# Performance work log

Measured on AMD Instinct MI355X. Metric: run time of the kernel, lower is better.

Reference implementation:

```python
import jax, jax.numpy as jnp
import numpy as np

N, E = 20000, 160000
F, H, OUT = 256, 8, 128
L = 6            # total layers -> 5 GAT layers
LM1 = L - 1
NGN = L // 3 + 1 # 3 GraphNorms
D = F // H       # 32 per head
GN_FREQ = 3
EPS = 1e-5


def setup_inputs() -> dict:
    key = jax.random.key(0)
    ks = jax.random.split(key, 12)
    x = jax.random.normal(ks[0], (N, 1), dtype=jnp.float32)
    edge_index = jax.random.randint(ks[1], (2, E), 0, N, dtype=jnp.int32)
    W0 = jax.random.normal(ks[2], (1, F), dtype=jnp.float32) * 0.1
    b0 = jnp.zeros((F,), jnp.float32)
    gat_lin = jax.random.normal(ks[3], (LM1, F, F), dtype=jnp.float32) * (1.0 / np.sqrt(F))
    att_src = jax.random.normal(ks[4], (LM1, H, D), dtype=jnp.float32) * 0.1
    att_dst = jax.random.normal(ks[5], (LM1, H, D), dtype=jnp.float32) * 0.1
    gat_bias = jnp.zeros((LM1, F), jnp.float32)
    gn_weight = jnp.ones((NGN, F), jnp.float32)
    gn_bias = jnp.zeros((NGN, F), jnp.float32)
    gn_mean_scale = jnp.ones((NGN, F), jnp.float32)
    lin_W = jax.random.normal(ks[6], (F, OUT), dtype=jnp.float32) * (1.0 / np.sqrt(F))
    lin_b = jnp.zeros((OUT,), jnp.float32)
    return {"x": x, "W0": W0, "b0": b0, "gat_lin": gat_lin, "att_src": att_src,
            "att_dst": att_dst, "gat_bias": gat_bias, "gn_weight": gn_weight,
            "gn_bias": gn_bias, "gn_mean_scale": gn_mean_scale,
            "lin_W": lin_W, "lin_b": lin_b, "edge_index": edge_index}


def _gcn_conv(x, W, b, src, dst, n):
    h = x @ W
    deg = jax.ops.segment_sum(jnp.ones(src.shape[0], h.dtype), dst, num_segments=n)
    dinv = jnp.where(deg > 0, jax.lax.rsqrt(deg), 0.0)
    norm = dinv[src] * dinv[dst]                      # [E']
    out = jax.ops.segment_sum(h[src] * norm[:, None], dst, num_segments=n)
    return out + b


def _gat_conv(x, W, a_src, a_dst, src, dst, n):
    # PyG GATConv (concat=True, negative_slope=0.2, self-loops in src/dst)
    h = (x @ W).reshape(n, H, D)
    s = jnp.einsum('nhd,hd->nh', h, a_src)            # [N,H]
    t = jnp.einsum('nhd,hd->nh', h, a_dst)
    e = jax.nn.leaky_relu(s[src] + t[dst], 0.2)       # [E',H]
    m = jax.ops.segment_max(e, dst, num_segments=n)   # per-dst softmax
    e = jnp.exp(e - m[dst])
    denom = jax.ops.segment_sum(e, dst, num_segments=n)
    alpha = e / (denom[dst] + 1e-16)
    out = jax.ops.segment_sum(h[src] * alpha[:, :, None], dst, num_segments=n)
    return out.reshape(n, F)


def _graph_norm(x, w, b, ms):
    # PyG GraphNorm with batch=None (single graph): per-feature stats over nodes
    mean = jnp.mean(x, axis=0)
    out = x - ms * mean
    var = jnp.mean(out * out, axis=0)
    return w * out * jax.lax.rsqrt(var + EPS) + b


def reference(x, W0, b0, gat_lin, att_src, att_dst, gat_bias, gn_weight, gn_bias,
              gn_mean_scale, lin_W, lin_b, edge_index):
    n = x.shape[0]
    loops = jnp.arange(n, dtype=edge_index.dtype)
    src = jnp.concatenate([edge_index[0], loops])
    dst = jnp.concatenate([edge_index[1], loops])
    h = jax.nn.relu(_gcn_conv(x, W0, b0, src, dst, n))
    for i in range(LM1):
        if i % GN_FREQ == 0:
            g = i // GN_FREQ
            h = _graph_norm(h, gn_weight[g], gn_bias[g], gn_mean_scale[g])
        out = _gat_conv(h, gat_lin[i], att_src[i], att_dst[i], src, dst, n)
        if i % GN_FREQ == 0:
            out = out + gat_bias[i]
        h = h + jax.nn.relu(out)
    return h @ lin_W + lin_b
```

## Files before the change

### kernel.cpp

```cpp
#include <hip/hip_runtime.h>
#include <hip/hip_bf16.h>
#include <stdint.h>

typedef float f32x4 __attribute__((ext_vector_type(4)));
typedef short s16x8 __attribute__((ext_vector_type(8)));

__device__ __forceinline__ float bf2f(unsigned short u) {
    union { unsigned int i; float f; } v; v.i = ((unsigned int)u) << 16; return v.f;
}
__device__ __forceinline__ unsigned short f2bf(float f) {
    union { float f; unsigned int i; } v; v.f = f;
    unsigned int x = v.i;
    return (unsigned short)((x + 0x7fffu + ((x >> 16) & 1u)) >> 16);
}
__device__ __forceinline__ void gload16(const void* g, void* l) {
    __builtin_amdgcn_global_load_lds(
        (const __attribute__((address_space(1))) void*)g,
        (__attribute__((address_space(3))) void*)l, 16, 0, 0);
}

__global__ void k_count(const int* __restrict__ ei, int E, int* deg) {
    int e = blockIdx.x * blockDim.x + threadIdx.x;
    if (e < E) atomicAdd(&deg[ei[E + e]], 1);
}

__global__ __launch_bounds__(256) void k_bsum(const int* __restrict__ deg,
                                              int* __restrict__ bsum, int n) {
    __shared__ int buf[256];
    int i = blockIdx.x * 256 + threadIdx.x;
    buf[threadIdx.x] = (i < n) ? deg[i] + 1 : 0;
    __syncthreads();
#pragma unroll
    for (int off = 128; off > 0; off >>= 1) {
        if ((int)threadIdx.x < off) buf[threadIdx.x] += buf[threadIdx.x + off];
        __syncthreads();
    }
    if (threadIdx.x == 0) bsum[blockIdx.x] = buf[0];
}

__global__ __launch_bounds__(256) void k_scanb(const int* __restrict__ bsum,
                                               int* __restrict__ boff, int nb) {
    __shared__ int buf[256];
    int t = threadIdx.x;
    int v = (t < nb) ? bsum[t] : 0;
    buf[t] = v;
    __syncthreads();
    for (int off = 1; off < 256; off <<= 1) {
        int add = (t >= off) ? buf[t - off] : 0;
        __syncthreads();
        buf[t] += add;
        __syncthreads();
    }
    if (t < nb) boff[t] = buf[t] - v;
}

__global__ __launch_bounds__(256) void k_emit(const int* __restrict__ deg,
                                              const int* __restrict__ boff,
                                              int* __restrict__ rowptr,
                                              int* __restrict__ wo,
                                              float* __restrict__ dinv, int n) {
    __shared__ int buf[256];
    int i = blockIdx.x * 256 + threadIdx.x;
    int v = (i < n) ? deg[i] + 1 : 0;
    buf[threadIdx.x] = v;
    __syncthreads();
    for (int off = 1; off < 256; off <<= 1) {
        int add = ((int)threadIdx.x >= off) ? buf[threadIdx.x - off] : 0;
        __syncthreads();
        buf[threadIdx.x] += add;
        __syncthreads();
    }
    if (i < n) {
        int excl = boff[blockIdx.x] + buf[threadIdx.x] - v;
        rowptr[i] = excl;
        wo[i] = excl;
        dinv[i] = rsqrtf((float)v);
        if (i == n - 1) rowptr[n] = excl + v;
    }
}

__global__ void k_fill(const int* __restrict__ ei, int E, int n,
                       int* wo, int* srcs) {
    int e = blockIdx.x * blockDim.x + threadIdx.x;
    int EP = E + n;
    if (e >= EP) return;
    int s_, d_;
    if (e < E) { s_ = ei[e]; d_ = ei[E + e]; }
    else       { s_ = d_ = e - E; }
    int pos = atomicAdd(&wo[d_], 1);
    srcs[pos] = s_;
}

__global__ __launch_bounds__(256) void k_h0f(const float* __restrict__ x,
                                             const float* __restrict__ dinv,
                                             const int* __restrict__ rowptr,
                                             const int* __restrict__ srcs,
                                             const float* __restrict__ W0,
                                             const float* __restrict__ b0,
                                             unsigned short* __restrict__ hbf,
                                             int n, int Mpad) {
    int wave = threadIdx.x >> 6, lane = threadIdx.x & 63;
    int node = blockIdx.x * 4 + wave;
    if (node >= Mpad) return;
    size_t base = (size_t)node * 256 + lane * 4;
    if (node >= n) {
        ushort4 z = {0, 0, 0, 0};
        *reinterpret_cast<ushort4*>(hbf + base) = z;
        return;
    }
    int p0 = rowptr[node], p1 = rowptr[node + 1];
    float sum = 0.f;
    for (int p = p0 + lane; p < p1; p += 64) {
        int s = srcs[p];
        sum += x[s] * dinv[s];
    }
#pragma unroll
    for (int m = 1; m < 64; m <<= 1) sum += __shfl_xor(sum, m);
    float sv = sum * dinv[node];
    float4 wv = *reinterpret_cast<const float4*>(W0 + lane * 4);
    float4 bv = *reinterpret_cast<const float4*>(b0 + lane * 4);
    ushort4 o;
    o.x = f2bf(fmaxf(sv * wv.x + bv.x, 0.f));
    o.y = f2bf(fmaxf(sv * wv.y + bv.y, 0.f));
    o.z = f2bf(fmaxf(sv * wv.z + bv.z, 0.f));
    o.w = f2bf(fmaxf(sv * wv.w + bv.w, 0.f));
    *reinterpret_cast<ushort4*>(hbf + base) = o;
}

__global__ void k_wprep(const float* __restrict__ gat_lin,
                        const float* __restrict__ lin_W,
                        const float* __restrict__ att_src,
                        const float* __restrict__ att_dst,
                        unsigned short* __restrict__ Wt,
                        unsigned short* __restrict__ lt) {
    int idx = blockIdx.x * blockDim.x + threadIdx.x;
    const int T1 = 5 * 65536;
    const int T2 = T1 + 128 * 256;
    const int T3 = T2 + 5 * 64 * 256;
    if (idx < T1) {
        int l = idx >> 16, r = idx & 0xFFFF;
        int nrow = r >> 8, k = r & 255;
        Wt[(size_t)l * 81920 + nrow * 256 + k] =
            f2bf(gat_lin[(size_t)l * 65536 + k * 256 + nrow]);
    } else if (idx < T2) {
        int j = idx - T1;
        int nrow = j >> 8, k = j & 255;
        lt[nrow * 256 + k] = f2bf(lin_W[(size_t)k * 128 + nrow]);
    } else if (idx < T3) {
        int j = idx - T2;
        int l = j >> 14, r = j & 16383;
        int row = r >> 8, k = r & 255;
        float v = 0.f;
        if (row < 16) {
            int head = row & 7;
            const float* a = (row < 8) ? (att_src + l * 256 + head * 32)
                                       : (att_dst + l * 256 + head * 32);
            const float* wr = gat_lin + (size_t)l * 65536 + k * 256 + head * 32;
#pragma unroll
            for (int d = 0; d < 32; ++d) v += wr[d] * a[d];
        }
        Wt[(size_t)l * 81920 + (256 + row) * 256 + k] = f2bf(v);
    }
}

__global__ __launch_bounds__(256) void k_gn_reduce(const unsigned short* __restrict__ hbf,
                                                   float* sums, float* sumsq, int n) {
    int f = threadIdx.x;
    float s = 0.f, q = 0.f;
    for (int r = blockIdx.x; r < n; r += gridDim.x) {
        float v = bf2f(hbf[(size_t)r * 256 + f]);
        s += v; q += v * v;
    }
    atomicAdd(&sums[f], s);
    atomicAdd(&sumsq[f], q);
}

__global__ __launch_bounds__(256) void k_gnfold(const float* __restrict__ st,
                                                const float* __restrict__ w,
                                                const float* __restrict__ b,
                                                const float* __restrict__ ms,
                                                unsigned short* __restrict__ Wt,
                                                float* __restrict__ so,
                                                float* __restrict__ rowbias,
                                                float ninv) {
    __shared__ float red[256];
    int col = blockIdx.x, k = threadIdx.x;
    float mean = st[k] * ninv;
    float m2   = st[256 + k] * ninv;
    float msf  = ms[k];
    float var  = m2 + msf * mean * mean * (msf - 2.0f);
    float sc = w[k] * rsqrtf(var + 1e-5f);
    float of = b[k] - msf * mean * sc;
    size_t idx = (size_t)col * 256 + k;
    float wv = bf2f(Wt[idx]);
    red[k] = of * wv;
    __syncthreads();
#pragma unroll
    for (int off = 128; off > 0; off >>= 1) {
        if (k < off) red[k] += red[k + off];
        __syncthreads();
    }
    if (k == 0) rowbias[col] = red[0];
    Wt[idx] = f2bf(sc * wv);
    if (col == 0) { so[k] = sc; so[256 + k] = of; }
}

#define BM 64
__global__ __launch_bounds__(512) void k_gemm_mfma(
    const unsigned short* __restrict__ A,
    const unsigned short* __restrict__ Bt,
    unsigned short* __restrict__ Cb,
    float* __restrict__ Cf,
    float* __restrict__ sbuf,
    float* __restrict__ tbuf,
    const float* __restrict__ bias,
    const float* __restrict__ rowbias,
    int M, int ldc, int nbTot, int nbPerY)
{
    __shared__ unsigned short As[64 * 256];
    __shared__ unsigned short Bs[2][64 * 256];
    const int tid = threadIdx.x;
    const int bm = blockIdx.x * BM;
    const int nb0 = blockIdx.y * nbPerY;
    int nb1 = nb0 + nbPerY; if (nb1 > nbTot) nb1 = nbTot;

    {
        const char* ga = (const char*)(A + (size_t)bm * 256);
        const char* gb = (const char*)(Bt + (size_t)nb0 * 16384);
        char* la = (char*)As;
        char* lb = (char*)Bs[0];
#pragma unroll
        for (int i = 0; i < 4; ++i) {
            int o  = (i * 512 + tid) * 16;
            int so = o ^ (((o >> 9) & 7) << 4);
            gload16(ga + so, la + o);
            gload16(gb + so, lb + o);
        }
    }
    __syncthreads();

    const int lane = tid & 63;
    const int w  = tid >> 6;
    const int wm = (w >> 1) * 16;
    const int wn = (w & 1) * 32;
    const int r  = lane & 15, kb = lane >> 4;
    const int r4 = (lane >> 4) * 4, cc = lane & 15;
    const char* la = (const char*)As;

    for (int nb = nb0; nb < nb1; ++nb) {
        int cur = (nb - nb0) & 1;
        if (nb + 1 < nb1) {
            const char* gb = (const char*)(Bt + (size_t)(nb + 1) * 16384);
            char* lb = (char*)Bs[cur ^ 1];
#pragma unroll
            for (int i = 0; i < 4; ++i) {
                int o  = (i * 512 + tid) * 16;
                int so = o ^ (((o >> 9) & 7) << 4);
                gload16(gb + so, lb + o);
            }
        }
        const char* lb = (const char*)Bs[cur];
        f32x4 acc[2] = {};
#pragma unroll
        for (int ks = 0; ks < 8; ++ks) {
            int row = wm + r;
            int c16 = (ks * 4 + kb) ^ (row & 7);
            s16x8 af = *(const s16x8*)(la + row * 512 + c16 * 16);
#pragma unroll
            for (int j = 0; j < 2; ++j) {
                int col = wn + j * 16 + r;
                int d16 = (ks * 4 + kb) ^ (col & 7);
                s16x8 bfr = *(const s16x8*)(lb + col * 512 + d16 * 16);
                acc[j] = __builtin_amdgcn_mfma_f32_16x16x32_bf16(af, bfr, acc[j], 0, 0, 0);
            }
        }
#pragma unroll
        for (int j = 0; j < 2; ++j) {
            int col = nb * 64 + wn + j * 16 + cc;
            float rb = rowbias ? rowbias[col] : 0.f;
#pragma unroll
            for (int q = 0; q < 4; ++q) {
                int row = bm + wm + r4 + q;
                float v = acc[j][q] + rb;
                if (Cb) {
                    if (col < 256) {
                        Cb[(size_t)row * 256 + col] = f2bf(v);
                    } else if (col < 264) {
                        sbuf[(size_t)row * 8 + (col - 256)] = v;
                    } else if (col < 272) {
                        tbuf[(size_t)row * 8 + (col - 264)] = v;
                    }
                } else if (row < M) {
                    Cf[(size_t)row * ldc + col] = v + bias[col];
                }
            }
        }
        __syncthreads();
    }
}

__global__ __launch_bounds__(256) void k_fagg(const unsigned short* __restrict__ h1,
                                              const float* __restrict__ sbuf,
                                              const float* __restrict__ tbuf,
                                              const int* __restrict__ rowptr,
                                              const int* __restrict__ srcs,
                                              unsigned short* __restrict__ hbf,
                                              const float* __restrict__ bias,
                                              const float* __restrict__ so, int n) {
    int wave = threadIdx.x >> 6, lane = threadIdx.x & 63;
    int node = blockIdx.x * 4 + wave;
    if (node >= n) return;
    int p0 = rowptr[node], p1 = rowptr[node + 1];
    int head = lane >> 3;
    float tv = tbuf[node * 8 + head];
    float m = -1e30f, den = 0.f;
    float a0 = 0.f, a1 = 0.f, a2 = 0.f, a3 = 0.f;
    int p = p0;
    for (; p + 3 < p1; p += 4) {
        int s0 = srcs[p], s1 = srcs[p + 1], s2 = srcs[p + 2], s3 = srcs[p + 3];
        float e0 = sbuf[s0 * 8 + head] + tv;
        float e1 = sbuf[s1 * 8 + head] + tv;
        float e2 = sbuf[s2 * 8 + head] + tv;
        float e3 = sbuf[s3 * 8 + head] + tv;
        ushort4 v0 = reinterpret_cast<const ushort4*>(h1 + (size_t)s0 * 256)[lane];
        ushort4 v1 = reinterpret_cast<const ushort4*>(h1 + (size_t)s1 * 256)[lane];
        ushort4 v2 = reinterpret_cast<const ushort4*>(h1 + (size_t)s2 * 256)[lane];
        ushort4 v3 = reinterpret_cast<const ushort4*>(h1 + (size_t)s3 * 256)[lane];
        e0 = (e0 > 0.f) ? e0 : 0.2f * e0;
        e1 = (e1 > 0.f) ? e1 : 0.2f * e1;
        e2 = (e2 > 0.f) ? e2 : 0.2f * e2;
        e3 = (e3 > 0.f) ? e3 : 0.2f * e3;
        float em = fmaxf(fmaxf(e0, e1), fmaxf(e2, e3));
        float mn = fmaxf(m, em);
        float sc = __expf(m - mn);
        float w0 = __expf(e0 - mn), w1 = __expf(e1 - mn);
        float w2 = __expf(e2 - mn), w3 = __expf(e3 - mn);
        den = den * sc + ((w0 + w1) + (w2 + w3));
        a0 = fmaf(a0, sc, w0 * bf2f(v0.x) + w1 * bf2f(v1.x) + w2 * bf2f(v2.x) + w3 * bf2f(v3.x));
        a1 = fmaf(a1, sc, w0 * bf2f(v0.y) + w1 * bf2f(v1.y) + w2 * bf2f(v2.y) + w3 * bf2f(v3.y));
        a2 = fmaf(a2, sc, w0 * bf2f(v0.z) + w1 * bf2f(v1.z) + w2 * bf2f(v2.z) + w3 * bf2f(v3.z));
        a3 = fmaf(a3, sc, w0 * bf2f(v0.w) + w1 * bf2f(v1.w) + w2 * bf2f(v2.w) + w3 * bf2f(v3.w));
        m = mn;
    }
    for (; p < p1; ++p) {
        int s0 = srcs[p];
        float e0 = sbuf[s0 * 8 + head] + tv;
        e0 = (e0 > 0.f) ? e0 : 0.2f * e0;
        ushort4 v0 = reinterpret_cast<const ushort4*>(h1 + (size_t)s0 * 256)[lane];
        float mn = fmaxf(m, e0);
        float sc = __expf(m - mn);
        float w0 = __expf(e0 - mn);
        den = den * sc + w0;
        a0 = fmaf(a0, sc, w0 * bf2f(v0.x));
        a1 = fmaf(a1, sc, w0 * bf2f(v0.y));
        a2 = fmaf(a2, sc, w0 * bf2f(v0.z));
        a3 = fmaf(a3, sc, w0 * bf2f(v0.w));
        m = mn;
    }
    float inv = 1.0f / (den + 1e-16f);
    a0 *= inv; a1 *= inv; a2 *= inv; a3 *= inv;
    float b0_ = 0.f, b1_ = 0.f, b2_ = 0.f, b3_ = 0.f;
    if (bias) {
        float4 bb = reinterpret_cast<const float4*>(bias)[lane];
        b0_ = bb.x; b1_ = bb.y; b2_ = bb.z; b3_ = bb.w;
    }
    size_t base = (size_t)node * 256 + lane * 4;
    ushort4 hv = *reinterpret_cast<const ushort4*>(hbf + base);
    float h0 = bf2f(hv.x), h1v = bf2f(hv.y), h2 = bf2f(hv.z), h3 = bf2f(hv.w);
    if (so) {
        float4 sc4 = reinterpret_cast<const float4*>(so)[lane];
        float4 of4 = reinterpret_cast<const float4*>(so + 256)[lane];
        h0 = h0 * sc4.x + of4.x; h1v = h1v * sc4.y + of4.y;
        h2 = h2 * sc4.z + of4.z; h3 = h3 * sc4.w + of4.w;
    }
    ushort4 o;
    o.x = f2bf(h0  + fmaxf(a0 + b0_, 0.f));
    o.y = f2bf(h1v + fmaxf(a1 + b1_, 0.f));
    o.z = f2bf(h2  + fmaxf(a2 + b2_, 0.f));
    o.w = f2bf(h3  + fmaxf(a3 + b3_, 0.f));
    *reinterpret_cast<ushort4*>(hbf + base) = o;
}

extern "C" void kernel_launch(void* const* d_in, const int* in_sizes, int n_in,
                              void* d_out, int out_size, void* d_ws, size_t ws_size,
                              hipStream_t stream) {
    const float* x        = (const float*)d_in[0];
    const float* W0       = (const float*)d_in[1];
    const float* b0       = (const float*)d_in[2];
    const float* gat_lin  = (const float*)d_in[3];
    const float* att_src  = (const float*)d_in[4];
    const float* att_dst  = (const float*)d_in[5];
    const float* gat_bias = (const float*)d_in[6];
    const float* gn_w     = (const float*)d_in[7];
    const float* gn_b     = (const float*)d_in[8];
    const float* gn_ms    = (const float*)d_in[9];
    const float* lin_W    = (const float*)d_in[10];
    const float* lin_b    = (const float*)d_in[11];
    const int*   ei       = (const int*)d_in[12];

    const int n  = in_sizes[0];
    const int E  = in_sizes[12] / 2;
    const int EP = E + n;
    const int Mpad = ((n + BM - 1) / BM) * BM;
    const int nb = (n + 255) / 256;

    char* w = (char*)d_ws;
    unsigned short* hbf = (unsigned short*)w; w += (size_t)Mpad * 256 * 2;
    unsigned short* h1  = (unsigned short*)w; w += (size_t)Mpad * 256 * 2;
    float* sbuf = (float*)w;                  w += (size_t)Mpad * 8 * 4;
    float* tbuf = (float*)w;                  w += (size_t)Mpad * 8 * 4;
    unsigned short* Wt = (unsigned short*)w;  w += (size_t)5 * 320 * 256 * 2;
    unsigned short* lt = (unsigned short*)w;  w += (size_t)128 * 256 * 2;
    float* scaleoff = (float*)w;              w += 1024 * 4;
    float* rowbias  = (float*)w;              w += 640 * 4;
    float* gnstat = (float*)w;                w += 1024 * 4;
    int* deg    = (int*)w;                    w += (size_t)n * 4;
    float* dinv = (float*)w;                  w += (size_t)n * 4;
    int* rowptr = (int*)w;                    w += ((size_t)(n + 1) * 4 + 15) / 16 * 16;
    int* wo     = (int*)w;                    w += (size_t)n * 4;
    int* bsum   = (int*)w;                    w += ((size_t)nb * 4 + 15) / 16 * 16;
    int* boff   = (int*)w;                    w += ((size_t)nb * 4 + 15) / 16 * 16;
    int* srcs   = (int*)w;                    w += (size_t)EP * 4;

    const int B256 = 256;
    auto cdiv = [](int a, int b) { return (a + b - 1) / b; };

    hipMemsetAsync(gnstat, 0, 1024 * 4 + (size_t)n * 4, stream);

    const int WPREP = 5 * 65536 + 128 * 256 + 5 * 64 * 256;
    k_wprep<<<cdiv(WPREP, B256), B256, 0, stream>>>(gat_lin, lin_W, att_src, att_dst, Wt, lt);

    k_count<<<cdiv(E, B256), B256, 0, stream>>>(ei, E, deg);
    k_bsum<<<nb, 256, 0, stream>>>(deg, bsum, n);
    k_scanb<<<1, 256, 0, stream>>>(bsum, boff, nb);
    k_emit<<<nb, 256, 0, stream>>>(deg, boff, rowptr, wo, dinv, n);
    k_fill<<<cdiv(EP, B256), B256, 0, stream>>>(ei, E, n, wo, srcs);

    k_h0f<<<cdiv(Mpad, 4), 256, 0, stream>>>(x, dinv, rowptr, srcs, W0, b0, hbf, n, Mpad);

    const float ninv = 1.0f / (float)n;
    const int gx = Mpad / BM;

    for (int i = 0; i < 5; ++i) {
        const float* rb = nullptr;
        const float* so = nullptr;
        if (i % 3 == 0) {
            int g = i / 3;
            k_gn_reduce<<<256, 256, 0, stream>>>(hbf, gnstat + g * 512,
                                                 gnstat + g * 512 + 256, n);
            k_gnfold<<<320, 256, 0, stream>>>(gnstat + g * 512, gn_w + g * 256,
                                              gn_b + g * 256, gn_ms + g * 256,
                                              Wt + (size_t)i * 81920,
                                              scaleoff + g * 512, rowbias + g * 320, ninv);
            rb = rowbias + g * 320;
            so = scaleoff + g * 512;
        }
        k_gemm_mfma<<<dim3(gx, 2), 512, 0, stream>>>(
            hbf, Wt + (size_t)i * 81920, h1, nullptr, sbuf, tbuf, nullptr, rb,
            n, 256, 5, 3);
        k_fagg<<<cdiv(n, 4), 256, 0, stream>>>(
            h1, sbuf, tbuf, rowptr, srcs, hbf,
            (i % 3 == 0) ? gat_bias + i * 256 : nullptr, so, n);
    }

    k_gemm_mfma<<<dim3(gx, 1), 512, 0, stream>>>(
        hbf, lt, nullptr, (float*)d_out, nullptr, nullptr, lin_b, nullptr,
        n, 128, 2, 2);
}
```

Before: 309.1 us.

## Split GEMM into one N-tile per block and halve-wave edge split in aggregation

The GEMM now gives each block a single 64-column output tile via a larger grid, which removes the double-buffered B loop and halves B's LDS footprint. That brings more parallelism and occupancy at the cost of reloading the A tile once per column tile. The aggregation kernel splits each node's edges across the two half-waves. Each lane loads 16 bytes (8 bf16) per edge, and the two halves merge their online-softmax state with cross-lane shuffles. This gives more independent gathers in flight and wider loads, but half the lanes sit idle during the epilogue.

```diff
diff --git a/kernel.cpp b/kernel.cpp
--- a/kernel.cpp
+++ b/kernel.cpp
@@ -12,6 +12,11 @@
     union { float f; unsigned int i; } v; v.f = f;
     unsigned int x = v.i;
     return (unsigned short)((x + 0x7fffu + ((x >> 16) & 1u)) >> 16);
+}
+__device__ __forceinline__ void bfp(unsigned int u, float& lo, float& hi) {
+    union { unsigned int i; float f; } a, b;
+    a.i = u << 16; b.i = u & 0xffff0000u;
+    lo = a.f; hi = b.f;
 }
 __device__ __forceinline__ void gload16(const void* g, void* l) {
     __builtin_amdgcn_global_load_lds(
@@ -215,20 +220,18 @@
     float* __restrict__ tbuf,
     const float* __restrict__ bias,
     const float* __restrict__ rowbias,
-    int M, int ldc, int nbTot, int nbPerY)
+    int M, int ldc)
 {
     __shared__ unsigned short As[64 * 256];
-    __shared__ unsigned short Bs[2][64 * 256];
+    __shared__ unsigned short Bs[64 * 256];
     const int tid = threadIdx.x;
     const int bm = blockIdx.x * BM;
-    const int nb0 = blockIdx.y * nbPerY;
-    int nb1 = nb0 + nbPerY; if (nb1 > nbTot) nb1 = nbTot;
-
+    const int bn = blockIdx.y * 64;
     {
         const char* ga = (const char*)(A + (size_t)bm * 256);
-        const char* gb = (const char*)(Bt + (size_t)nb0 * 16384);
+        const char* gb = (const char*)(Bt + (size_t)bn * 256);
         char* la = (char*)As;
-        char* lb = (char*)Bs[0];
+        char* lb = (char*)Bs;
 #pragma unroll
         for (int i = 0; i < 4; ++i) {
             int o  = (i * 512 + tid) * 16;
@@ -246,56 +249,42 @@
     const int r  = lane & 15, kb = lane >> 4;
     const int r4 = (lane >> 4) * 4, cc = lane & 15;
     const char* la = (const char*)As;
-
-    for (int nb = nb0; nb < nb1; ++nb) {
-        int cur = (nb - nb0) & 1;
-        if (nb + 1 < nb1) {
-            const char* gb = (const char*)(Bt + (size_t)(nb + 1) * 16384);
-            char* lb = (char*)Bs[cur ^ 1];
-#pragma unroll
-            for (int i = 0; i < 4; ++i) {
-                int o  = (i * 512 + tid) * 16;
-                int so = o ^ (((o >> 9) & 7) << 4);
-                gload16(gb + so, lb + o);
+    const char* lb = (const char*)Bs;
+
+    f32x4 acc[2] = {};
+#pragma unroll
+    for (int ks = 0; ks < 8; ++ks) {
+        int row = wm + r;
+        int c16 = (ks * 4 + kb) ^ (row & 7);
+        s16x8 af = *(const s16x8*)(la + row * 512 + c16 * 16);
+#pragma unroll
+        for (int j = 0; j < 2; ++j) {
+            int col = wn + j * 16 + r;
+            int d16 = (ks * 4 + kb) ^ (col & 7);
+            s16x8 bfr = *(const s16x8*)(lb + col * 512 + d16 * 16);
+            acc[j] = __builtin_amdgcn_mfma_f32_16x16x32_bf16(af, bfr, acc[j], 0, 0, 0);
+        }
+    }
+#pragma unroll
+    for (int j = 0; j < 2; ++j) {
+        int col = bn + wn + j * 16 + cc;
+        float rb = rowbias ? rowbias[col] : 0.f;
+#pragma unroll
+        for (int q = 0; q < 4; ++q) {
+            int row = bm + wm + r4 + q;
+            float v = acc[j][q] + rb;
+            if (Cb) {
+                if (col < 256) {
+                    Cb[(size_t)row * 256 + col] = f2bf(v);
+                } else if (col < 264) {
+                    sbuf[(size_t)row * 8 + (col - 256)] = v;
+                } else if (col < 272) {
+                    tbuf[(size_t)row * 8 + (col - 264)] = v;
+                }
+            } else if (row < M) {
+                Cf[(size_t)row * ldc + col] = v + bias[col];
             }
         }
-        const char* lb = (const char*)Bs[cur];
-        f32x4 acc[2] = {};
-#pragma unroll
-        for (int ks = 0; ks < 8; ++ks) {
-            int row = wm + r;
-            int c16 = (ks * 4 + kb) ^ (row & 7);
-            s16x8 af = *(const s16x8*)(la + row * 512 + c16 * 16);
-#pragma unroll
-            for (int j = 0; j < 2; ++j) {
-                int col = wn + j * 16 + r;
-                int d16 = (ks * 4 + kb) ^ (col & 7);
-                s16x8 bfr = *(const s16x8*)(lb + col * 512 + d16 * 16);
-                acc[j] = __builtin_amdgcn_mfma_f32_16x16x32_bf16(af, bfr, acc[j], 0, 0, 0);
-            }
-        }
-#pragma unroll
-        for (int j = 0; j < 2; ++j) {
-            int col = nb * 64 + wn + j * 16 + cc;
-            float rb = rowbias ? rowbias[col] : 0.f;
-#pragma unroll
-            for (int q = 0; q < 4; ++q) {
-                int row = bm + wm + r4 + q;
-                float v = acc[j][q] + rb;
-                if (Cb) {
-                    if (col < 256) {
-                        Cb[(size_t)row * 256 + col] = f2bf(v);
-                    } else if (col < 264) {
-                        sbuf[(size_t)row * 8 + (col - 256)] = v;
-                    } else if (col < 272) {
-                        tbuf[(size_t)row * 8 + (col - 264)] = v;
-                    }
-                } else if (row < M) {
-                    Cf[(size_t)row * ldc + col] = v + bias[col];
-                }
-            }
-        }
-        __syncthreads();
     }
 }
 
@@ -311,74 +300,114 @@
     int node = blockIdx.x * 4 + wave;
     if (node >= n) return;
     int p0 = rowptr[node], p1 = rowptr[node + 1];
-    int head = lane >> 3;
+    int hid = lane >> 5;
+    int l5 = lane & 31;
+    int fl = l5 * 8;
+    int head = l5 >> 2;
     float tv = tbuf[node * 8 + head];
     float m = -1e30f, den = 0.f;
     float a0 = 0.f, a1 = 0.f, a2 = 0.f, a3 = 0.f;
-    int p = p0;
-    for (; p + 3 < p1; p += 4) {
-        int s0 = srcs[p], s1 = srcs[p + 1], s2 = srcs[p + 2], s3 = srcs[p + 3];
+    float a4 = 0.f, a5 = 0.f, a6 = 0.f, a7 = 0.f;
+    int q = p0 + hid;
+    for (; q + 2 < p1; q += 4) {
+        int s0 = srcs[q], s1 = srcs[q + 2];
         float e0 = sbuf[s0 * 8 + head] + tv;
         float e1 = sbuf[s1 * 8 + head] + tv;
-        float e2 = sbuf[s2 * 8 + head] + tv;
-        float e3 = sbuf[s3 * 8 + head] + tv;
-        ushort4 v0 = reinterpret_cast<const ushort4*>(h1 + (size_t)s0 * 256)[lane];
-        ushort4 v1 = reinterpret_cast<const ushort4*>(h1 + (size_t)s1 * 256)[lane];
-        ushort4 v2 = reinterpret_cast<const ushort4*>(h1 + (size_t)s2 * 256)[lane];
-        ushort4 v3 = reinterpret_cast<const ushort4*>(h1 + (size_t)s3 * 256)[lane];
+        uint4 v0 = *reinterpret_cast<const uint4*>(h1 + (size_t)s0 * 256 + fl);
+        uint4 v1 = *reinterpret_cast<const uint4*>(h1 + (size_t)s1 * 256 + fl);
         e0 = (e0 > 0.f) ? e0 : 0.2f * e0;
         e1 = (e1 > 0.f) ? e1 : 0.2f * e1;
-        e2 = (e2 > 0.f) ? e2 : 0.2f * e2;
-        e3 = (e3 > 0.f) ? e3 : 0.2f * e3;
-        float em = fmaxf(fmaxf(e0, e1), fmaxf(e2, e3));
-        float mn = fmaxf(m, em);
+        float mn = fmaxf(m, fmaxf(e0, e1));
         float sc = __expf(m - mn);
         float w0 = __expf(e0 - mn), w1 = __expf(e1 - mn);
-        float w2 = __expf(e2 - mn), w3 = __expf(e3 - mn);
-        den = den * sc + ((w0 + w1) + (w2 + w3));
-        a0 = fmaf(a0, sc, w0 * bf2f(v0.x) + w1 * bf2f(v1.x) + w2 * bf2f(v2.x) + w3 * bf2f(v3.x));
-        a1 = fmaf(a1, sc, w0 * bf2f(v0.y) + w1 * bf2f(v1.y) + w2 * bf2f(v2.y) + w3 * bf2f(v3.y));
-        a2 = fmaf(a2, sc, w0 * bf2f(v0.z) + w1 * bf2f(v1.z) + w2 * bf2f(v2.z) + w3 * bf2f(v3.z));
-        a3 = fmaf(a3, sc, w0 * bf2f(v0.w) + w1 * bf2f(v1.w) + w2 * bf2f(v2.w) + w3 * bf2f(v3.w));
+        den = den * sc + (w0 + w1);
+        float f0l, f0h, f1l, f1h;
+        bfp(v0.x, f0l, f0h); bfp(v1.x, f1l, f1h);
+        a0 = fmaf(a0, sc, w0 * f0l + w1 * f1l);
+        a1 = fmaf(a1, sc, w0 * f0h + w1 * f1h);
+        bfp(v0.y, f0l, f0h); bfp(v1.y, f1l, f1h);
+        a2 = fmaf(a2, sc, w0 * f0l + w1 * f1l);
+        a3 = fmaf(a3, sc, w0 * f0h + w1 * f1h);
+        bfp(v0.z, f0l, f0h); bfp(v1.z, f1l, f1h);
+        a4 = fmaf(a4, sc, w0 * f0l + w1 * f1l);
+        a5 = fmaf(a5, sc, w0 * f0h + w1 * f1h);
+        bfp(v0.w, f0l, f0h); bfp(v1.w, f1l, f1h);
+        a6 = fmaf(a6, sc, w0 * f0l + w1 * f1l);
+        a7 = fmaf(a7, sc, w0 * f0h + w1 * f1h);
         m = mn;
     }
-    for (; p < p1; ++p) {
-        int s0 = srcs[p];
+    for (; q < p1; q += 2) {
+        int s0 = srcs[q];
         float e0 = sbuf[s0 * 8 + head] + tv;
+        uint4 v0 = *reinterpret_cast<const uint4*>(h1 + (size_t)s0 * 256 + fl);
         e0 = (e0 > 0.f) ? e0 : 0.2f * e0;
-        ushort4 v0 = reinterpret_cast<const ushort4*>(h1 + (size_t)s0 * 256)[lane];
         float mn = fmaxf(m, e0);
         float sc = __expf(m - mn);
         float w0 = __expf(e0 - mn);
         den = den * sc + w0;
-        a0 = fmaf(a0, sc, w0 * bf2f(v0.x));
-        a1 = fmaf(a1, sc, w0 * bf2f(v0.y));
-        a2 = fmaf(a2, sc, w0 * bf2f(v0.z));
-        a3 = fmaf(a3, sc, w0 * bf2f(v0.w));
+        float f0l, f0h;
+        bfp(v0.x, f0l, f0h);
+        a0 = fmaf(a0, sc, w0 * f0l); a1 = fmaf(a1, sc, w0 * f0h);
+        bfp(v0.y, f0l, f0h);
+        a2 = fmaf(a2, sc, w0 * f0l); a3 = fmaf(a3, sc, w0 * f0h);
+        bfp(v0.z, f0l, f0h);
+        a4 = fmaf(a4, sc, w0 * f0l); a5 = fmaf(a5, sc, w0 * f0h);
+        bfp(v0.w, f0l, f0h);
+        a6 = fmaf(a6, sc, w0 * f0l); a7 = fmaf(a7, sc, w0 * f0h);
         m = mn;
     }
+    float mo = __shfl_xor(m, 32);
+    float mm = fmaxf(m, mo);
+    float sc = __expf(m - mm);
+    den *= sc; den += __shfl_xor(den, 32);
+    a0 *= sc; a0 += __shfl_xor(a0, 32);
+    a1 *= sc; a1 += __shfl_xor(a1, 32);
+    a2 *= sc; a2 += __shfl_xor(a2, 32);
+    a3 *= sc; a3 += __shfl_xor(a3, 32);
+    a4 *= sc; a4 += __shfl_xor(a4, 32);
+    a5 *= sc; a5 += __shfl_xor(a5, 32);
+    a6 *= sc; a6 += __shfl_xor(a6, 32);
+    a7 *= sc; a7 += __shfl_xor(a7, 32);
+    if (hid) return;
     float inv = 1.0f / (den + 1e-16f);
     a0 *= inv; a1 *= inv; a2 *= inv; a3 *= inv;
-    float b0_ = 0.f, b1_ = 0.f, b2_ = 0.f, b3_ = 0.f;
+    a4 *= inv; a5 *= inv; a6 *= inv; a7 *= inv;
+    float b_[8] = {0.f, 0.f, 0.f, 0.f, 0.f, 0.f, 0.f, 0.f};
     if (bias) {
-        float4 bb = reinterpret_cast<const float4*>(bias)[lane];
-        b0_ = bb.x; b1_ = bb.y; b2_ = bb.z; b3_ = bb.w;
-    }
-    size_t base = (size_t)node * 256 + lane * 4;
-    ushort4 hv = *reinterpret_cast<const ushort4*>(hbf + base);
-    float h0 = bf2f(hv.x), h1v = bf2f(hv.y), h2 = bf2f(hv.z), h3 = bf2f(hv.w);
+        float4 blo = *reinterpret_cast<const float4*>(bias + fl);
+        float4 bhi = *reinterpret_cast<const float4*>(bias + fl + 4);
+        b_[0] = blo.x; b_[1] = blo.y; b_[2] = blo.z; b_[3] = blo.w;
+        b_[4] = bhi.x; b_[5] = bhi.y; b_[6] = bhi.z; b_[7] = bhi.w;
+    }
+    size_t base = (size_t)node * 256 + fl;
+    uint4 hv = *reinterpret_cast<const uint4*>(hbf + base);
+    float h_[8];
+    bfp(hv.x, h_[0], h_[1]); bfp(hv.y, h_[2], h_[3]);
+    bfp(hv.z, h_[4], h_[5]); bfp(hv.w, h_[6], h_[7]);
     if (so) {
-        float4 sc4 = reinterpret_cast<const float4*>(so)[lane];
-        float4 of4 = reinterpret_cast<const float4*>(so + 256)[lane];
-        h0 = h0 * sc4.x + of4.x; h1v = h1v * sc4.y + of4.y;
-        h2 = h2 * sc4.z + of4.z; h3 = h3 * sc4.w + of4.w;
-    }
-    ushort4 o;
-    o.x = f2bf(h0  + fmaxf(a0 + b0_, 0.f));
-    o.y = f2bf(h1v + fmaxf(a1 + b1_, 0.f));
-    o.z = f2bf(h2  + fmaxf(a2 + b2_, 0.f));
-    o.w = f2bf(h3  + fmaxf(a3 + b3_, 0.f));
-    *reinterpret_cast<ushort4*>(hbf + base) = o;
+        float4 s0v = *reinterpret_cast<const float4*>(so + fl);
+        float4 s1v = *reinterpret_cast<const float4*>(so + fl + 4);
+        float4 o0v = *reinterpret_cast<const float4*>(so + 256 + fl);
+        float4 o1v = *reinterpret_cast<const float4*>(so + 256 + fl + 4);
+        h_[0] = h_[0] * s0v.x + o0v.x; h_[1] = h_[1] * s0v.y + o0v.y;
+        h_[2] = h_[2] * s0v.z + o0v.z; h_[3] = h_[3] * s0v.w + o0v.w;
+        h_[4] = h_[4] * s1v.x + o1v.x; h_[5] = h_[5] * s1v.y + o1v.y;
+        h_[6] = h_[6] * s1v.z + o1v.z; h_[7] = h_[7] * s1v.w + o1v.w;
+    }
+    float r0 = h_[0] + fmaxf(a0 + b_[0], 0.f);
+    float r1 = h_[1] + fmaxf(a1 + b_[1], 0.f);
+    float r2 = h_[2] + fmaxf(a2 + b_[2], 0.f);
+    float r3 = h_[3] + fmaxf(a3 + b_[3], 0.f);
+    float r4 = h_[4] + fmaxf(a4 + b_[4], 0.f);
+    float r5 = h_[5] + fmaxf(a5 + b_[5], 0.f);
+    float r6 = h_[6] + fmaxf(a6 + b_[6], 0.f);
+    float r7 = h_[7] + fmaxf(a7 + b_[7], 0.f);
+    uint4 o;
+    o.x = (unsigned int)f2bf(r0) | ((unsigned int)f2bf(r1) << 16);
+    o.y = (unsigned int)f2bf(r2) | ((unsigned int)f2bf(r3) << 16);
+    o.z = (unsigned int)f2bf(r4) | ((unsigned int)f2bf(r5) << 16);
+    o.w = (unsigned int)f2bf(r6) | ((unsigned int)f2bf(r7) << 16);
+    *reinterpret_cast<uint4*>(hbf + base) = o;
 }
 
 extern "C" void kernel_launch(void* const* d_in, const int* in_sizes, int n_in,
@@ -455,15 +484,15 @@
             rb = rowbias + g * 320;
             so = scaleoff + g * 512;
         }
-        k_gemm_mfma<<<dim3(gx, 2), 512, 0, stream>>>(
+        k_gemm_mfma<<<dim3(gx, 5), 512, 0, stream>>>(
             hbf, Wt + (size_t)i * 81920, h1, nullptr, sbuf, tbuf, nullptr, rb,
-            n, 256, 5, 3);
+            n, 256);
         k_fagg<<<cdiv(n, 4), 256, 0, stream>>>(
             h1, sbuf, tbuf, rowptr, srcs, hbf,
             (i % 3 == 0) ? gat_bias + i * 256 : nullptr, so, n);
     }
 
-    k_gemm_mfma<<<dim3(gx, 1), 512, 0, stream>>>(
+    k_gemm_mfma<<<dim3(gx, 2), 512, 0, stream>>>(
         hbf, lt, nullptr, (float*)d_out, nullptr, nullptr, lin_b, nullptr,
-        n, 128, 2, 2);
-}
+        n, 128);
+}
```

Result: faster. 286.7 us (-7.3%).
